# Kernel tuning notes

Hardware: AMD Instinct MI355X
Metric: run time of the kernel (lower is better)

Reference implementation:

```python
import jax, jax.numpy as jnp
import numpy as np

EPS = 1e-5
K = 3
K2 = K * K


def _conv(x, w, pad=0):
    return jax.lax.conv_general_dilated(
        x, w, (1, 1), [(pad, pad), (pad, pad)],
        dimension_numbers=('NCHW', 'OIHW', 'NCHW'))


def _bn_silu(x, gamma, beta, mean, var):
    scale = (gamma / jnp.sqrt(var + EPS))[None, :, None, None]
    y = (x - mean[None, :, None, None]) * scale + beta[None, :, None, None]
    return y * jax.nn.sigmoid(y)  # SiLU


def _space_to_depth(x, s=2):
    b, c, h, w = x.shape
    x = x.reshape(b, c, h // s, s, w // s, s)
    x = x.transpose(0, 1, 3, 5, 2, 4)
    return x.reshape(b, c * s * s, h // s, w // s)


def _deform_sample(x, offset, mask, pad=1):
    # x: (B,C,H,W); offset: (B,2*K2,H,W) layout [kk -> (dy,dx)]; mask: (B,K2,H,W)
    B, C, H, W = x.shape
    off = offset.reshape(B, K2, 2, H, W)
    oy, ox = off[:, :, 0], off[:, :, 1]
    ki = jnp.repeat(jnp.arange(K), K)  # kernel row (y), (K2,)
    kj = jnp.tile(jnp.arange(K), K)    # kernel col (x), (K2,)
    base_y = (jnp.arange(H)[None, :, None] - pad + ki[:, None, None]).astype(x.dtype)  # (K2,H,1)
    base_x = (jnp.arange(W)[None, None, :] - pad + kj[:, None, None]).astype(x.dtype)  # (K2,1,W)
    py = base_y[None] + oy  # (B,K2,H,W)
    px = base_x[None] + ox

    y0 = jnp.floor(py)
    x0 = jnp.floor(px)
    wy = py - y0
    wx = px - x0
    y0i = y0.astype(jnp.int32)
    x0i = x0.astype(jnp.int32)

    xf = x.reshape(B, C, H * W)
    gather = jax.vmap(lambda a, i: a[:, i])  # (C,HW),(N)->(C,N)

    out = jnp.zeros((B, C, K2, H, W), x.dtype)
    for dy in (0, 1):
        for dx in (0, 1):
            yi = y0i + dy
            xi = x0i + dx
            valid = (yi >= 0) & (yi < H) & (xi >= 0) & (xi < W)
            w = (wy if dy else 1.0 - wy) * (wx if dx else 1.0 - wx) * valid
            idx = (jnp.clip(yi, 0, H - 1) * W + jnp.clip(xi, 0, W - 1)).reshape(B, -1)
            vals = gather(xf, idx).reshape(B, C, K2, H, W)
            out = out + vals * w[:, None]
    return out * mask[:, None]  # modulated


def setup_inputs() -> dict:
    key = jax.random.key(0)
    ks = jax.random.split(key, 12)
    B, C1, H, W = 8, 128, 160, 160
    C_SPD, C_MID, C2 = C1 * 4, 128, 256
    inp = {
        'x': jax.random.normal(ks[0], (B, C1, H, W), jnp.float32),
        'reduce_w': jax.random.normal(ks[1], (C_MID, C_SPD, 1, 1), jnp.float32) * 0.05,
        'reduce_gamma': jax.random.uniform(ks[2], (C_MID,), jnp.float32, 0.5, 1.5),
        'reduce_beta': jax.random.normal(ks[3], (C_MID,), jnp.float32) * 0.1,
        'reduce_mean': jax.random.normal(ks[4], (C_MID,), jnp.float32) * 0.1,
        'reduce_var': jax.random.uniform(ks[5], (C_MID,), jnp.float32, 0.5, 1.5),
        'off_w': jax.random.normal(ks[6], (27, C_MID, 3, 3), jnp.float32) * 0.01,
        'off_b': jnp.zeros((27,), jnp.float32),
        'dcn_w': jax.random.normal(ks[7], (C2, C_MID, 3, 3), jnp.float32) * 0.03,
        'dcn_gamma': jax.random.uniform(ks[8], (C2,), jnp.float32, 0.5, 1.5),
        'dcn_beta': jax.random.normal(ks[9], (C2,), jnp.float32) * 0.1,
        'dcn_mean': jax.random.normal(ks[10], (C2,), jnp.float32) * 0.1,
        'dcn_var': jax.random.uniform(ks[11], (C2,), jnp.float32, 0.5, 1.5),
    }
    return inp


def reference(x, reduce_w, reduce_gamma, reduce_beta, reduce_mean, reduce_var,
              off_w, off_b, dcn_w, dcn_gamma, dcn_beta, dcn_mean, dcn_var):
    # SPD: (B,C,H,W) -> (B,4C,H/2,W/2)
    x = _space_to_depth(x, 2)
    # 1x1 reduce + BN + SiLU
    x = _bn_silu(_conv(x, reduce_w), reduce_gamma, reduce_beta, reduce_mean, reduce_var)
    # offset/mask prediction (3x3 conv, pad=1)
    om = _conv(x, off_w, pad=1) + off_b[None, :, None, None]
    offset = om[:, :2 * K2]
    mask = jax.nn.sigmoid(om[:, 2 * K2:3 * K2])
    # modulated deformable 3x3 conv (stride 1, pad 1)
    samp = _deform_sample(x, offset, mask, pad=1)  # (B,C_mid,9,H,W)
    O = dcn_w.shape[0]
    out = jnp.einsum('bckhw,ock->bohw', samp, dcn_w.reshape(O, dcn_w.shape[1], K2))
    return _bn_silu(out, dcn_gamma, dcn_beta, dcn_mean, dcn_var)
```

## Files before the change

kernel.cpp:

```cpp
#include <hip/hip_runtime.h>

constexpr int HW  = 6400;
constexpr int WW  = 80;

typedef __attribute__((ext_vector_type(8))) short short8;
typedef __attribute__((ext_vector_type(4))) float f32x4;
typedef unsigned short ushort_t;

__device__ __forceinline__ float sigmoidf_(float x) { return 1.f / (1.f + __expf(-x)); }
__device__ __forceinline__ float siluf_(float y) { return y / (1.f + __expf(-y)); }
__device__ __forceinline__ ushort_t f2bf(float f) {
    unsigned u = __float_as_uint(f);
    u += 0x7FFFu + ((u >> 16) & 1u);
    return (ushort_t)(u >> 16);
}
__device__ __forceinline__ float bf2f(ushort_t h) {
    return __uint_as_float(((unsigned)h) << 16);
}

__global__ __launch_bounds__(256) void k0_prep(
    const float* __restrict__ rw, const float* __restrict__ ow,
    const float* __restrict__ dw,
    const float* __restrict__ rg, const float* __restrict__ rb,
    const float* __restrict__ rm, const float* __restrict__ rv,
    ushort_t* __restrict__ WB,
    ushort_t* __restrict__ WoB, ushort_t* __restrict__ WdB,
    float* __restrict__ scr, float* __restrict__ shr)
{
    const int i = blockIdx.x * 256 + threadIdx.x;
    if (blockIdx.x == 0 && threadIdx.x < 128) {
        const int m = threadIdx.x;
        const float sc = rg[m] * rsqrtf(rv[m] + 1e-5f);
        scr[m] = sc;
        shr[m] = rb[m] - rm[m] * sc;
    }
    if (i < 65536) {
        const int e = i & 7;
        const int lane = (i >> 3) & 63;
        const int chunkW = i >> 9;
        const int nt = chunkW >> 4, kks = chunkW & 15;
        const int kk = kks * 32 + ((lane >> 4) << 3) + e;
        const int o = (nt << 4) + (lane & 15);
        WB[i] = f2bf(rw[o * 512 + kk]);
    }
    const int j = i - 65536;
    if (j >= 0 && j < 36864) {
        const int e = j & 7;
        const int lane = (j >> 3) & 63;
        const int chunk = j >> 9;
        const int nf = chunk / 36, ksg = chunk % 36;
        const int kk = ksg * 32 + ((lane >> 4) << 3) + e;
        const int q = kk >> 7, c = kk & 127;
        const int o = (nf << 4) + (lane & 15);
        WoB[j] = (o < 27) ? f2bf(ow[o * 1152 + c * 9 + q]) : (ushort_t)0;
    }
    const int l = j - 36864;
    if (l >= 0 && l < 294912) {
        const int e = l & 7;
        const int lane = (l >> 3) & 63;
        const int chunk = l >> 9;
        const int ot = chunk / 36, ksg = chunk % 36;
        const int kk = ksg * 32 + ((lane >> 4) << 3) + e;
        const int tap = kk >> 7, c = kk & 127;
        const int o = (ot << 4) + (lane & 15);
        WdB[l] = f2bf(dw[o * 1152 + c * 9 + tap]);
    }
}

__global__ __launch_bounds__(256) void k1_reduce(
    const float* __restrict__ x,
    const ushort_t* __restrict__ WB,
    const float* __restrict__ scr, const float* __restrict__ shr,
    ushort_t* __restrict__ xm_bf)
{
    const int t    = threadIdx.x;
    const int lane = t & 63;
    const int wave = t >> 6;
    const int q = lane >> 4, ln = lane & 15;
    const int p0 = blockIdx.x * 64;
    const int bb = p0 / HW;
    const int px = wave * 16 + ln;
    const int hw = (p0 % HW) + px;
    const int h = hw / WW, w = hw % WW;
    const float* xb = x + (size_t)bb * 128 * 25600 + (2 * h) * 160 + 2 * w;

    f32x4 acc[8] = {};

#pragma unroll 4
    for (int kks = 0; kks < 16; ++kks) {
        const int c0 = kks * 8 + q * 2;
        const float* pc0 = xb + (size_t)c0 * 25600;
        const float* pc1 = pc0 + 25600;
        const float2 a0 = *reinterpret_cast<const float2*>(pc0);
        const float2 a1 = *reinterpret_cast<const float2*>(pc0 + 160);
        const float2 b0 = *reinterpret_cast<const float2*>(pc1);
        const float2 b1 = *reinterpret_cast<const float2*>(pc1 + 160);
        short8 p;
        p[0] = (short)f2bf(a0.x); p[1] = (short)f2bf(a0.y);
        p[2] = (short)f2bf(a1.x); p[3] = (short)f2bf(a1.y);
        p[4] = (short)f2bf(b0.x); p[5] = (short)f2bf(b0.y);
        p[6] = (short)f2bf(b1.x); p[7] = (short)f2bf(b1.y);
#pragma unroll
        for (int nt = 0; nt < 8; ++nt) {
            const short8 wf = *reinterpret_cast<const short8*>(WB + ((nt << 4) + kks) * 512 + lane * 8);
            acc[nt] = __builtin_amdgcn_mfma_f32_16x16x32_bf16(wf, p, acc[nt], 0, 0, 0);
        }
    }

    const int pi = p0 + px;
    ushort_t* op = xm_bf + (size_t)pi * 128;
#pragma unroll
    for (int nt = 0; nt < 8; ++nt) {
        const int ob = nt * 16 + q * 4;
        const float4 s4 = *reinterpret_cast<const float4*>(scr + ob);
        const float4 b4 = *reinterpret_cast<const float4*>(shr + ob);
        const float y0 = siluf_(acc[nt][0] * s4.x + b4.x);
        const float y1 = siluf_(acc[nt][1] * s4.y + b4.y);
        const float y2 = siluf_(acc[nt][2] * s4.z + b4.z);
        const float y3 = siluf_(acc[nt][3] * s4.w + b4.w);
        *reinterpret_cast<uint2*>(op + ob) =
            make_uint2(f2bf(y0) | ((unsigned)f2bf(y1) << 16),
                       f2bf(y2) | ((unsigned)f2bf(y3) << 16));
    }
}

__global__ __launch_bounds__(256) void k2_off(
    const ushort_t* __restrict__ xm_bf, const ushort_t* __restrict__ WoB,
    const float* __restrict__ obias, float* __restrict__ om)
{
    __shared__ __align__(16) ushort_t A[2][64 * 128];
    __shared__ __align__(16) float T[32 * 64];

    const int t = threadIdx.x;
    const int lane = t & 63;
    const int wave = t >> 6;
    const int p0 = blockIdx.x * 64;
    const int bb = p0 / HW;
    const int hw0 = p0 % HW;

    const int spx = t & 63;
    const int hws = hw0 + spx;
    const int hh = hws / WW, wwp = hws % WW;

    auto STAGE = [&](int q, int buf) {
        const int dy = q / 3 - 1, dx = q % 3 - 1;
        const int y = hh + dy, xx = wwp + dx;
        const bool valid = ((unsigned)y < 80u) && ((unsigned)xx < 80u);
        const ushort_t* src = xm_bf + ((size_t)bb * HW + y * WW + xx) * 128 + wave * 32;
#pragma unroll
        for (int s = 0; s < 4; ++s) {
            uint4 v = make_uint4(0u, 0u, 0u, 0u);
            if (valid) v = *reinterpret_cast<const uint4*>(src + s * 8);
            const int cslot = wave * 4 + s;
            *reinterpret_cast<uint4*>(&A[buf][spx * 128 + ((cslot ^ (spx & 7)) << 3)]) = v;
        }
    };

    const int q4 = lane >> 4, ln = lane & 15;
    f32x4 acc[2] = {};

    auto GEMM = [&](int q, int buf) {
#pragma unroll
        for (int ks = 0; ks < 4; ++ks) {
            const int px = wave * 16 + ln;
            const int elem = px * 128 + (((ks * 4 + q4) ^ (px & 7)) << 3);
            const short8 a = *reinterpret_cast<const short8*>(&A[buf][elem]);
#pragma unroll
            for (int nf = 0; nf < 2; ++nf) {
                const int chunk = nf * 36 + q * 4 + ks;
                const short8 b = *reinterpret_cast<const short8*>(WoB + chunk * 512 + lane * 8);
                acc[nf] = __builtin_amdgcn_mfma_f32_16x16x32_bf16(a, b, acc[nf], 0, 0, 0);
            }
        }
    };

    STAGE(0, 0);
    __syncthreads();
    for (int q = 0; q < 9; ++q) {
        if (q < 8) STAGE(q + 1, (q + 1) & 1);
        GEMM(q, q & 1);
        __syncthreads();
    }

#pragma unroll
    for (int nf = 0; nf < 2; ++nf)
#pragma unroll
        for (int r = 0; r < 4; ++r) {
            const int o = nf * 16 + ln;
            const int px = wave * 16 + q4 * 4 + r;
            T[o * 64 + px] = acc[nf][r];
        }
    __syncthreads();
    for (int i = t; i < 27 * 64; i += 256) {
        const int o = i >> 6, px = i & 63;
        om[((size_t)bb * 27 + o) * HW + hw0 + px] = T[i] + obias[o];
    }
}

__global__ __launch_bounds__(512) void k3_dcn(
    const ushort_t* __restrict__ xm_bf, const float* __restrict__ om,
    const ushort_t* __restrict__ WdB,
    const float* __restrict__ g, const float* __restrict__ be,
    const float* __restrict__ mu, const float* __restrict__ va,
    float* __restrict__ out)
{
    __shared__ __align__(16) ushort_t S[2][64 * 128];
    __shared__ __align__(16) float4 geoW[9][64];
    __shared__ __align__(16) int4   geoI[9][64];

    const int t    = threadIdx.x;
    const int lane = t & 63;
    const int wave = t >> 6;
    const int p0   = blockIdx.x * 64;
    const int bb   = p0 / HW;
    const int hw0  = p0 % HW;

    for (int it = t; it < 576; it += 512) {
        const int tap = it >> 6, px = it & 63;
        const int hw = hw0 + px;
        const int h = hw / WW, w = hw % WW;
        const float* ob = om + (size_t)bb * 27 * HW + hw;
        const float oy = ob[(2 * tap) * HW];
        const float ox = ob[(2 * tap + 1) * HW];
        const float mk = sigmoidf_(ob[(18 + tap) * HW]);
        float py  = (float)(h - 1 + tap / 3) + oy;
        float pxf = (float)(w - 1 + tap % 3) + ox;
        py  = fminf(fmaxf(py, -1000.f), 1000.f);
        pxf = fminf(fmaxf(pxf, -1000.f), 1000.f);
        const float fy = floorf(py), fx = floorf(pxf);
        const int y0 = (int)fy, x0 = (int)fx, y1 = y0 + 1, x1 = x0 + 1;
        const float wy = py - fy, wx = pxf - fx;
        const float vy0 = ((unsigned)y0 < 80u) ? 1.f : 0.f;
        const float vy1 = ((unsigned)y1 < 80u) ? 1.f : 0.f;
        const float vx0 = ((unsigned)x0 < 80u) ? 1.f : 0.f;
        const float vx1 = ((unsigned)x1 < 80u) ? 1.f : 0.f;
        float4 wv;
        wv.x = (1.f - wy) * (1.f - wx) * vy0 * vx0 * mk;
        wv.y = (1.f - wy) * wx * vy0 * vx1 * mk;
        wv.z = wy * (1.f - wx) * vy1 * vx0 * mk;
        wv.w = wy * wx * vy1 * vx1 * mk;
        const int cy0 = min(max(y0, 0), 79), cy1 = min(max(y1, 0), 79);
        const int cx0 = min(max(x0, 0), 79), cx1 = min(max(x1, 0), 79);
        int4 iv;
        iv.x = cy0 * WW + cx0; iv.y = cy0 * WW + cx1;
        iv.z = cy1 * WW + cx0; iv.w = cy1 * WW + cx1;
        geoW[tap][px] = wv;
        geoI[tap][px] = iv;
    }
    __syncthreads();

    const ushort_t* xb = xm_bf + (size_t)bb * HW * 128;

    const int spx = t >> 3;
    const int scg = t & 7;

    auto SAMPLE = [&](int tap, int bufIdx) {
        const float4 wv = geoW[tap][spx];
        const int4  iv = geoI[tap][spx];
        const uint4* c00 = reinterpret_cast<const uint4*>(xb + (size_t)iv.x * 128 + scg * 16);
        const uint4* c01 = reinterpret_cast<const uint4*>(xb + (size_t)iv.y * 128 + scg * 16);
        const uint4* c10 = reinterpret_cast<const uint4*>(xb + (size_t)iv.z * 128 + scg * 16);
        const uint4* c11 = reinterpret_cast<const uint4*>(xb + (size_t)iv.w * 128 + scg * 16);
#pragma unroll
        for (int half = 0; half < 2; ++half) {
            const uint4 a = c00[half], b = c01[half], c = c10[half], d = c11[half];
            const unsigned* ap = (const unsigned*)&a;
            const unsigned* bp = (const unsigned*)&b;
            const unsigned* cp = (const unsigned*)&c;
            const unsigned* dp = (const unsigned*)&d;
            unsigned pk[4];
#pragma unroll
            for (int u = 0; u < 4; ++u) {
                const float alo = __uint_as_float(ap[u] << 16), ahi = __uint_as_float(ap[u] & 0xFFFF0000u);
                const float blo = __uint_as_float(bp[u] << 16), bhi = __uint_as_float(bp[u] & 0xFFFF0000u);
                const float clo = __uint_as_float(cp[u] << 16), chi = __uint_as_float(cp[u] & 0xFFFF0000u);
                const float dlo = __uint_as_float(dp[u] << 16), dhi = __uint_as_float(dp[u] & 0xFFFF0000u);
                const float slo = wv.x * alo + wv.y * blo + wv.z * clo + wv.w * dlo;
                const float shi = wv.x * ahi + wv.y * bhi + wv.z * chi + wv.w * dhi;
                pk[u] = (unsigned)f2bf(slo) | ((unsigned)f2bf(shi) << 16);
            }
            const int cslot = scg * 2 + half;
            const int elem  = spx * 128 + ((cslot ^ (spx & 7)) << 3);
            *reinterpret_cast<uint4*>(&S[bufIdx][elem]) =
                make_uint4(pk[0], pk[1], pk[2], pk[3]);
        }
    };

    const int wM = wave >> 2, wN = wave & 3;
    const int q = lane >> 4, ln = lane & 15;
    f32x4 acc[2][4] = {};

    auto GEMM = [&](int tap, int bufIdx) {
#pragma unroll
        for (int ks = 0; ks < 4; ++ks) {
            short8 a0, a1;
            {
                const int px = wM * 32 + ln;
                const int elem = px * 128 + (((ks * 4 + q) ^ (px & 7)) << 3);
                a0 = *reinterpret_cast<const short8*>(&S[bufIdx][elem]);
            }
            {
                const int px = wM * 32 + 16 + ln;
                const int elem = px * 128 + (((ks * 4 + q) ^ (px & 7)) << 3);
                a1 = *reinterpret_cast<const short8*>(&S[bufIdx][elem]);
            }
#pragma unroll
            for (int nt = 0; nt < 4; ++nt) {
                const int ot = wN * 4 + nt;
                const int chunk = ot * 36 + tap * 4 + ks;
                const short8 b = *reinterpret_cast<const short8*>(WdB + chunk * 512 + lane * 8);
                acc[0][nt] = __builtin_amdgcn_mfma_f32_16x16x32_bf16(a0, b, acc[0][nt], 0, 0, 0);
                acc[1][nt] = __builtin_amdgcn_mfma_f32_16x16x32_bf16(a1, b, acc[1][nt], 0, 0, 0);
            }
        }
    };

    SAMPLE(0, 0);
    __syncthreads();
    for (int tap = 0; tap < 9; ++tap) {
        if (tap < 8) SAMPLE(tap + 1, (tap + 1) & 1);
        GEMM(tap, tap & 1);
        __syncthreads();
    }

    float sc[4], sh[4];
#pragma unroll
    for (int nt = 0; nt < 4; ++nt) {
        const int o = wN * 64 + nt * 16 + ln;
        sc[nt] = g[o] * rsqrtf(va[o] + 1e-5f);
        sh[nt] = be[o] - mu[o] * sc[nt];
    }
#pragma unroll
    for (int mt = 0; mt < 2; ++mt)
#pragma unroll
        for (int nt = 0; nt < 4; ++nt) {
            const int o = wN * 64 + nt * 16 + ln;
            float* obase = out + (size_t)bb * 256 * HW + (size_t)o * HW;
            float4 st;
            st.x = siluf_(acc[mt][nt][0] * sc[nt] + sh[nt]);
            st.y = siluf_(acc[mt][nt][1] * sc[nt] + sh[nt]);
            st.z = siluf_(acc[mt][nt][2] * sc[nt] + sh[nt]);
            st.w = siluf_(acc[mt][nt][3] * sc[nt] + sh[nt]);
            *reinterpret_cast<float4*>(obase + hw0 + wM * 32 + mt * 16 + q * 4) = st;
        }
}

extern "C" void kernel_launch(void* const* d_in, const int* in_sizes, int n_in,
                              void* d_out, int out_size, void* d_ws, size_t ws_size,
                              hipStream_t stream)
{
    const float* x        = (const float*)d_in[0];
    const float* reduce_w = (const float*)d_in[1];
    const float* rg       = (const float*)d_in[2];
    const float* rb       = (const float*)d_in[3];
    const float* rm       = (const float*)d_in[4];
    const float* rv       = (const float*)d_in[5];
    const float* off_w    = (const float*)d_in[6];
    const float* off_b    = (const float*)d_in[7];
    const float* dcn_w    = (const float*)d_in[8];
    const float* dg       = (const float*)d_in[9];
    const float* db       = (const float*)d_in[10];
    const float* dm       = (const float*)d_in[11];
    const float* dv       = (const float*)d_in[12];

    float* ws  = (float*)d_ws;
    ushort_t* xm_bf = (ushort_t*)ws;
    float* om   = ws + 3276800;
    ushort_t* WB   = (ushort_t*)(om + 1382400);
    ushort_t* WoB  = WB + 65536;
    ushort_t* WdB  = WoB + 36864;
    float* scr = (float*)(WdB + 294912);
    float* shr = scr + 128;

    k0_prep<<<dim3(1552), dim3(256), 0, stream>>>(reduce_w, off_w, dcn_w,
                                                  rg, rb, rm, rv,
                                                  WB, WoB, WdB, scr, shr);
    k1_reduce<<<dim3(800), dim3(256), 0, stream>>>(x, WB, scr, shr, xm_bf);
    k2_off<<<dim3(800), dim3(256), 0, stream>>>(xm_bf, WoB, off_b, om);
    k3_dcn<<<dim3(800), dim3(512), 0, stream>>>(xm_bf, om, WdB, dg, db, dm, dv, (float*)d_out);
}
```

Measured before the change: 194.9 us.

## Sample DCN operands directly into MFMA registers and remap blocks across XCDs

The deformable conv kernel no longer stages bilinear samples in shared memory with a double buffer and barriers. Each wave now gathers its own four corner vectors, blends them straight into MFMA A-operands, and covers 128 output channels with 256 threads instead of 512. Blocks in all three main kernels are also remapped so that neighbouring pixel tiles land on the same XCD, for L2 locality. The cost is duplicated gathers, since the two N-waves each sample the same pixels, plus higher register pressure from 16 accumulators per wave.

```diff
diff --git a/kernel.cpp b/kernel.cpp
--- a/kernel.cpp
+++ b/kernel.cpp
@@ -16,6 +16,29 @@
 }
 __device__ __forceinline__ float bf2f(ushort_t h) {
     return __uint_as_float(((unsigned)h) << 16);
+}
+__device__ __forceinline__ int xcd_bid800(int b) { return (b & 7) * 100 + (b >> 3); }
+
+__device__ __forceinline__ short8 blend8(const float4 w,
+    const uint4 A, const uint4 B, const uint4 C, const uint4 D)
+{
+    const unsigned* ap = (const unsigned*)&A;
+    const unsigned* bp = (const unsigned*)&B;
+    const unsigned* cp = (const unsigned*)&C;
+    const unsigned* dp = (const unsigned*)&D;
+    unsigned r[4];
+#pragma unroll
+    for (int u = 0; u < 4; ++u) {
+        const float alo = __uint_as_float(ap[u] << 16), ahi = __uint_as_float(ap[u] & 0xFFFF0000u);
+        const float blo = __uint_as_float(bp[u] << 16), bhi = __uint_as_float(bp[u] & 0xFFFF0000u);
+        const float clo = __uint_as_float(cp[u] << 16), chi = __uint_as_float(cp[u] & 0xFFFF0000u);
+        const float dlo = __uint_as_float(dp[u] << 16), dhi = __uint_as_float(dp[u] & 0xFFFF0000u);
+        const float slo = w.x * alo + w.y * blo + w.z * clo + w.w * dlo;
+        const float shi = w.x * ahi + w.y * bhi + w.z * chi + w.w * dhi;
+        r[u] = (unsigned)f2bf(slo) | ((unsigned)f2bf(shi) << 16);
+    }
+    uint4 pk = make_uint4(r[0], r[1], r[2], r[3]);
+    return *reinterpret_cast<short8*>(&pk);
 }
 
 __global__ __launch_bounds__(256) void k0_prep(
@@ -77,7 +100,7 @@
     const int lane = t & 63;
     const int wave = t >> 6;
     const int q = lane >> 4, ln = lane & 15;
-    const int p0 = blockIdx.x * 64;
+    const int p0 = xcd_bid800(blockIdx.x) * 64;
     const int bb = p0 / HW;
     const int px = wave * 16 + ln;
     const int hw = (p0 % HW) + px;
@@ -134,7 +157,7 @@
     const int t = threadIdx.x;
     const int lane = t & 63;
     const int wave = t >> 6;
-    const int p0 = blockIdx.x * 64;
+    const int p0 = xcd_bid800(blockIdx.x) * 64;
     const int bb = p0 / HW;
     const int hw0 = p0 % HW;
 
@@ -197,25 +220,25 @@
     }
 }
 
-__global__ __launch_bounds__(512) void k3_dcn(
+__global__ __launch_bounds__(256, 4) void k3_dcn(
     const ushort_t* __restrict__ xm_bf, const float* __restrict__ om,
     const ushort_t* __restrict__ WdB,
     const float* __restrict__ g, const float* __restrict__ be,
     const float* __restrict__ mu, const float* __restrict__ va,
     float* __restrict__ out)
 {
-    __shared__ __align__(16) ushort_t S[2][64 * 128];
     __shared__ __align__(16) float4 geoW[9][64];
     __shared__ __align__(16) int4   geoI[9][64];
 
     const int t    = threadIdx.x;
     const int lane = t & 63;
-    const int wave = t >> 6;
-    const int p0   = blockIdx.x * 64;
+    const int wv   = t >> 6;
+    const int wM   = wv >> 1, wN = wv & 1;
+    const int p0   = xcd_bid800(blockIdx.x) * 64;
     const int bb   = p0 / HW;
     const int hw0  = p0 % HW;
 
-    for (int it = t; it < 576; it += 512) {
+    for (int it = t; it < 576; it += 256) {
         const int tap = it >> 6, px = it & 63;
         const int hw = hw0 + px;
         const int h = hw / WW, w = hw % WW;
@@ -234,115 +257,73 @@
         const float vy1 = ((unsigned)y1 < 80u) ? 1.f : 0.f;
         const float vx0 = ((unsigned)x0 < 80u) ? 1.f : 0.f;
         const float vx1 = ((unsigned)x1 < 80u) ? 1.f : 0.f;
-        float4 wv;
-        wv.x = (1.f - wy) * (1.f - wx) * vy0 * vx0 * mk;
-        wv.y = (1.f - wy) * wx * vy0 * vx1 * mk;
-        wv.z = wy * (1.f - wx) * vy1 * vx0 * mk;
-        wv.w = wy * wx * vy1 * vx1 * mk;
+        float4 wvv;
+        wvv.x = (1.f - wy) * (1.f - wx) * vy0 * vx0 * mk;
+        wvv.y = (1.f - wy) * wx * vy0 * vx1 * mk;
+        wvv.z = wy * (1.f - wx) * vy1 * vx0 * mk;
+        wvv.w = wy * wx * vy1 * vx1 * mk;
         const int cy0 = min(max(y0, 0), 79), cy1 = min(max(y1, 0), 79);
         const int cx0 = min(max(x0, 0), 79), cx1 = min(max(x1, 0), 79);
         int4 iv;
         iv.x = cy0 * WW + cx0; iv.y = cy0 * WW + cx1;
         iv.z = cy1 * WW + cx0; iv.w = cy1 * WW + cx1;
-        geoW[tap][px] = wv;
+        geoW[tap][px] = wvv;
         geoI[tap][px] = iv;
     }
     __syncthreads();
 
     const ushort_t* xb = xm_bf + (size_t)bb * HW * 128;
-
-    const int spx = t >> 3;
-    const int scg = t & 7;
-
-    auto SAMPLE = [&](int tap, int bufIdx) {
-        const float4 wv = geoW[tap][spx];
-        const int4  iv = geoI[tap][spx];
-        const uint4* c00 = reinterpret_cast<const uint4*>(xb + (size_t)iv.x * 128 + scg * 16);
-        const uint4* c01 = reinterpret_cast<const uint4*>(xb + (size_t)iv.y * 128 + scg * 16);
-        const uint4* c10 = reinterpret_cast<const uint4*>(xb + (size_t)iv.z * 128 + scg * 16);
-        const uint4* c11 = reinterpret_cast<const uint4*>(xb + (size_t)iv.w * 128 + scg * 16);
-#pragma unroll
-        for (int half = 0; half < 2; ++half) {
-            const uint4 a = c00[half], b = c01[half], c = c10[half], d = c11[half];
-            const unsigned* ap = (const unsigned*)&a;
-            const unsigned* bp = (const unsigned*)&b;
-            const unsigned* cp = (const unsigned*)&c;
-            const unsigned* dp = (const unsigned*)&d;
-            unsigned pk[4];
-#pragma unroll
-            for (int u = 0; u < 4; ++u) {
-                const float alo = __uint_as_float(ap[u] << 16), ahi = __uint_as_float(ap[u] & 0xFFFF0000u);
-                const float blo = __uint_as_float(bp[u] << 16), bhi = __uint_as_float(bp[u] & 0xFFFF0000u);
-                const float clo = __uint_as_float(cp[u] << 16), chi = __uint_as_float(cp[u] & 0xFFFF0000u);
-                const float dlo = __uint_as_float(dp[u] << 16), dhi = __uint_as_float(dp[u] & 0xFFFF0000u);
-                const float slo = wv.x * alo + wv.y * blo + wv.z * clo + wv.w * dlo;
-                const float shi = wv.x * ahi + wv.y * bhi + wv.z * chi + wv.w * dhi;
-                pk[u] = (unsigned)f2bf(slo) | ((unsigned)f2bf(shi) << 16);
-            }
-            const int cslot = scg * 2 + half;
-            const int elem  = spx * 128 + ((cslot ^ (spx & 7)) << 3);
-            *reinterpret_cast<uint4*>(&S[bufIdx][elem]) =
-                make_uint4(pk[0], pk[1], pk[2], pk[3]);
-        }
-    };
-
-    const int wM = wave >> 2, wN = wave & 3;
     const int q = lane >> 4, ln = lane & 15;
-    f32x4 acc[2][4] = {};
-
-    auto GEMM = [&](int tap, int bufIdx) {
+    const int pxl0 = wM * 32 + ln;
+    const int pxl1 = pxl0 + 16;
+
+    f32x4 acc[2][8] = {};
+
+    for (int tap = 0; tap < 9; ++tap) {
+        const int4  iv0 = geoI[tap][pxl0];
+        const int4  iv1 = geoI[tap][pxl1];
+        const float4 wv0 = geoW[tap][pxl0];
+        const float4 wv1 = geoW[tap][pxl1];
 #pragma unroll
         for (int ks = 0; ks < 4; ++ks) {
-            short8 a0, a1;
-            {
-                const int px = wM * 32 + ln;
-                const int elem = px * 128 + (((ks * 4 + q) ^ (px & 7)) << 3);
-                a0 = *reinterpret_cast<const short8*>(&S[bufIdx][elem]);
-            }
-            {
-                const int px = wM * 32 + 16 + ln;
-                const int elem = px * 128 + (((ks * 4 + q) ^ (px & 7)) << 3);
-                a1 = *reinterpret_cast<const short8*>(&S[bufIdx][elem]);
-            }
-#pragma unroll
-            for (int nt = 0; nt < 4; ++nt) {
-                const int ot = wN * 4 + nt;
+            const int co = (ks * 4 + q) * 8;
+            const uint4 c00 = *reinterpret_cast<const uint4*>(xb + (size_t)iv0.x * 128 + co);
+            const uint4 c01 = *reinterpret_cast<const uint4*>(xb + (size_t)iv0.y * 128 + co);
+            const uint4 c10 = *reinterpret_cast<const uint4*>(xb + (size_t)iv0.z * 128 + co);
+            const uint4 c11 = *reinterpret_cast<const uint4*>(xb + (size_t)iv0.w * 128 + co);
+            const uint4 d00 = *reinterpret_cast<const uint4*>(xb + (size_t)iv1.x * 128 + co);
+            const uint4 d01 = *reinterpret_cast<const uint4*>(xb + (size_t)iv1.y * 128 + co);
+            const uint4 d10 = *reinterpret_cast<const uint4*>(xb + (size_t)iv1.z * 128 + co);
+            const uint4 d11 = *reinterpret_cast<const uint4*>(xb + (size_t)iv1.w * 128 + co);
+            const short8 a0 = blend8(wv0, c00, c01, c10, c11);
+            const short8 a1 = blend8(wv1, d00, d01, d10, d11);
+#pragma unroll
+            for (int nt = 0; nt < 8; ++nt) {
+                const int ot = wN * 8 + nt;
                 const int chunk = ot * 36 + tap * 4 + ks;
                 const short8 b = *reinterpret_cast<const short8*>(WdB + chunk * 512 + lane * 8);
                 acc[0][nt] = __builtin_amdgcn_mfma_f32_16x16x32_bf16(a0, b, acc[0][nt], 0, 0, 0);
                 acc[1][nt] = __builtin_amdgcn_mfma_f32_16x16x32_bf16(a1, b, acc[1][nt], 0, 0, 0);
             }
         }
-    };
-
-    SAMPLE(0, 0);
-    __syncthreads();
-    for (int tap = 0; tap < 9; ++tap) {
-        if (tap < 8) SAMPLE(tap + 1, (tap + 1) & 1);
-        GEMM(tap, tap & 1);
-        __syncthreads();
-    }
-
-    float sc[4], sh[4];
-#pragma unroll
-    for (int nt = 0; nt < 4; ++nt) {
-        const int o = wN * 64 + nt * 16 + ln;
-        sc[nt] = g[o] * rsqrtf(va[o] + 1e-5f);
-        sh[nt] = be[o] - mu[o] * sc[nt];
-    }
-#pragma unroll
-    for (int mt = 0; mt < 2; ++mt)
-#pragma unroll
-        for (int nt = 0; nt < 4; ++nt) {
-            const int o = wN * 64 + nt * 16 + ln;
-            float* obase = out + (size_t)bb * 256 * HW + (size_t)o * HW;
+    }
+
+#pragma unroll
+    for (int nt = 0; nt < 8; ++nt) {
+        const int o = wN * 128 + nt * 16 + ln;
+        const float sc = g[o] * rsqrtf(va[o] + 1e-5f);
+        const float sh = be[o] - mu[o] * sc;
+        float* obase = out + (size_t)bb * 256 * HW + (size_t)o * HW;
+#pragma unroll
+        for (int mt = 0; mt < 2; ++mt) {
             float4 st;
-            st.x = siluf_(acc[mt][nt][0] * sc[nt] + sh[nt]);
-            st.y = siluf_(acc[mt][nt][1] * sc[nt] + sh[nt]);
-            st.z = siluf_(acc[mt][nt][2] * sc[nt] + sh[nt]);
-            st.w = siluf_(acc[mt][nt][3] * sc[nt] + sh[nt]);
+            st.x = siluf_(acc[mt][nt][0] * sc + sh);
+            st.y = siluf_(acc[mt][nt][1] * sc + sh);
+            st.z = siluf_(acc[mt][nt][2] * sc + sh);
+            st.w = siluf_(acc[mt][nt][3] * sc + sh);
             *reinterpret_cast<float4*>(obase + hw0 + wM * 32 + mt * 16 + q * 4) = st;
         }
+    }
 }
 
 extern "C" void kernel_launch(void* const* d_in, const int* in_sizes, int n_in,
@@ -377,5 +358,5 @@
                                                   WB, WoB, WdB, scr, shr);
     k1_reduce<<<dim3(800), dim3(256), 0, stream>>>(x, WB, scr, shr, xm_bf);
     k2_off<<<dim3(800), dim3(256), 0, stream>>>(xm_bf, WoB, off_b, om);
-    k3_dcn<<<dim3(800), dim3(512), 0, stream>>>(xm_bf, om, WdB, dg, db, dm, dv, (float*)d_out);
-}
+    k3_dcn<<<dim3(800), dim3(256), 0, stream>>>(xm_bf, om, WdB, dg, db, dm, dv, (float*)d_out);
+}
```

After: 524.4 us. 169% more time.
